# Kernel optimization log

Hardware: AMD Instinct MI355X
Metric: run time of the kernel (lower is better)

The kernel has to match this reference:

```python
import jax, jax.numpy as jnp
import numpy as np

N = 100000
D = 16          # input_dim
NUM_FILTERS = 8
NNZ = 1600000


def setup_inputs() -> dict:
    key = jax.random.key(0)
    k1, k2, k3, k4, k5 = jax.random.split(key, 5)
    x = jax.random.normal(k1, (N, D), dtype=jnp.float32)
    L_rows = jax.random.randint(k2, (NNZ,), 0, N, dtype=jnp.int64 if jax.config.jax_enable_x64 else jnp.int32).astype(jnp.int32)
    L_cols = jax.random.randint(k3, (NNZ,), 0, N, dtype=jnp.int32)
    L_v = jax.random.normal(k4, (NNZ,), dtype=jnp.float32)
    node_attr_eig = jax.random.uniform(k5, (N,), dtype=jnp.float32)
    return {"x": x, "L_rows": L_rows, "L_cols": L_cols, "L_v": L_v, "node_attr_eig": node_attr_eig}


def reference(x, L_rows, L_cols, L_v, node_attr_eig):
    n, d = x.shape
    f = NUM_FILTERS
    # exponents = 2 ** arange(num_filters + 1)
    exponents = (2 ** jnp.arange(f + 1)).astype(x.dtype)  # [F+1]
    # coeffs = x.T @ L  ==  (L.T @ x).T ; compute L.T @ x as [N, D]
    # (L.T @ x)[c] = sum over nnz entries (r, c): L_v * x[r]
    LTx = jax.ops.segment_sum(L_v[:, None] * x[L_rows], L_cols, num_segments=n)  # [N, D]
    # exponential eigenfilter bank: w = exp(-eig)^exponents, wavelet differences
    w = jnp.exp(-node_attr_eig)[:, None] ** exponents[None, :]  # [N, F+1]
    w_wav = w[:, :-1] - w[:, 1:]                                # [N, F]
    # g_eig = coeffs[..., None] * w_wav[None, ...] permuted to [N, D, F]
    g_eig = (LTx[:, :, None] * w_wav[:, None, :]).reshape(n, d * f)  # [N, D*F]
    # filtered = L @ g_eig : out[r] = sum over nnz (r, c): L_v * g_eig[c]
    out = jax.ops.segment_sum(L_v[:, None] * g_eig[L_cols], L_rows, num_segments=n)
    return out.reshape(n, d, f)
```

## Files before the change

### kernel.cpp

```cpp
#include <hip/hip_runtime.h>

#define N_NODES   100000
#define D_DIM     16
#define NFILT     8
#define KOUT      128
#define NNZ_CNT   1600000

#define CBITS     8
#define CROWS     256
#define NCB       ((N_NODES + CROWS - 1) / CROWS)
#define CAP       5120
#define EPB       4096
#define NBLKA     ((NNZ_CNT + EPB - 1) / EPB)

__device__ __forceinline__ uint f32_to_bf16_bits(float f) {
    uint u = __float_as_uint(f);
    uint r = (u + 0x7FFFu + ((u >> 16) & 1u)) >> 16;
    return r;
}

__global__ void wav_kernel(const float* __restrict__ eig, ushort* __restrict__ wavb) {
    int n = blockIdx.x * blockDim.x + threadIdx.x;
    if (n >= N_NODES) return;
    float cur = expf(-eig[n]);
    uint pk[4];
#pragma unroll
    for (int h = 0; h < 4; ++h) {
        float nx0 = cur * cur;
        float w0 = cur - nx0;
        float nx1 = nx0 * nx0;
        float w1 = nx0 - nx1;
        cur = nx1;
        pk[h] = f32_to_bf16_bits(w0) | (f32_to_bf16_bits(w1) << 16);
    }
    *(uint4*)(wavb + (size_t)n * NFILT) = make_uint4(pk[0], pk[1], pk[2], pk[3]);
}

__global__ void scatter1_kernel(const float* __restrict__ x,
                                const int* __restrict__ rows,
                                const int* __restrict__ cols,
                                const float* __restrict__ v,
                                float* __restrict__ LTxI) {
    long long idx = (long long)blockIdx.x * blockDim.x + threadIdx.x;
    if (idx >= (long long)NNZ_CNT * D_DIM) return;
    int e = (int)(idx >> 4);
    int d = (int)(idx & 15);
    int r = rows[e];
    int c = cols[e];
    float val = v[e] * x[(size_t)r * D_DIM + d];
    int slot = ((d & 7) << 1) + (d >> 3);
    atomicAdd(LTxI + (size_t)c * D_DIM + slot, val);
}

__global__ void pack_kernel(const float* __restrict__ LTxI, uint* __restrict__ LTxP) {
    int idx = blockIdx.x * blockDim.x + threadIdx.x;
    if (idx >= N_NODES * NFILT) return;
    float2 lp = *(const float2*)(LTxI + (size_t)idx * 2);
    LTxP[idx] = f32_to_bf16_bits(lp.x) | (f32_to_bf16_bits(lp.y) << 16);
}

__global__ __launch_bounds__(512) void binA_kernel(const int* __restrict__ rows,
                                                   const int* __restrict__ cols,
                                                   const float* __restrict__ v,
                                                   int* __restrict__ gcur,
                                                   int2* __restrict__ regA) {
    __shared__ int cnt[NCB];
    __shared__ int offb[NCB];
    __shared__ int gbase[NCB];
    __shared__ int sc[512];
    __shared__ int2 rec[EPB];
    int tid = threadIdx.x;
    int e0 = blockIdx.x * EPB;
    int nE = NNZ_CNT - e0; if (nE > EPB) nE = EPB;

    for (int i = tid; i < NCB; i += 512) cnt[i] = 0;
    __syncthreads();
    for (int i = tid; i < nE; i += 512)
        atomicAdd(&cnt[rows[e0 + i] >> CBITS], 1);
    __syncthreads();

    sc[tid] = (tid < NCB) ? cnt[tid] : 0;
    __syncthreads();
    for (int off = 1; off < 512; off <<= 1) {
        int t = (tid >= off) ? sc[tid - off] : 0;
        __syncthreads();
        sc[tid] += t;
        __syncthreads();
    }
    if (tid < NCB) {
        int cv = cnt[tid];
        int st = sc[tid] - cv;
        offb[tid] = st;
        gbase[tid] = cv ? atomicAdd(&gcur[tid], cv) : 0;
        cnt[tid] = st;
    }
    __syncthreads();

    for (int i = tid; i < nE; i += 512) {
        int r = rows[e0 + i], c = cols[e0 + i];
        float val = v[e0 + i];
        int b = r >> CBITS;
        int pos = atomicAdd(&cnt[b], 1);
        rec[pos] = make_int2(((r & (CROWS - 1)) << 17) | c, __float_as_int(val));
    }
    __syncthreads();

    int wv = tid >> 6, lane = tid & 63;
    for (int b = wv; b < NCB; b += 8) {
        int s = offb[b];
        int n = cnt[b] - s;
        size_t dst = (size_t)b * CAP + gbase[b];
        for (int i = lane; i < n; i += 64)
            regA[dst + i] = rec[s + i];
    }
}

__global__ __launch_bounds__(512) void binB_kernel(const int* __restrict__ gcur,
                                                   int2* __restrict__ regA,
                                                   int2* __restrict__ offs2) {
    __shared__ int2 rec[CAP];
    __shared__ int cnt[CROWS];
    __shared__ int sc[CROWS];
    int tid = threadIdx.x;
    int b = blockIdx.x;
    int nb = gcur[b]; if (nb > CAP) nb = CAP;
    size_t base = (size_t)b * CAP;

    if (tid < CROWS) cnt[tid] = 0;
    __syncthreads();
    for (int i = tid; i < nb; i += 512) {
        int2 r = regA[base + i];
        rec[i] = r;
        atomicAdd(&cnt[r.x >> 17], 1);
    }
    __syncthreads();

    int cv = (tid < CROWS) ? cnt[tid] : 0;
    if (tid < CROWS) sc[tid] = cv;
    __syncthreads();
    for (int off = 1; off < CROWS; off <<= 1) {
        int t = (tid < CROWS && tid >= off) ? sc[tid - off] : 0;
        __syncthreads();
        if (tid < CROWS) sc[tid] += t;
        __syncthreads();
    }
    if (tid < CROWS) {
        int st = sc[tid] - cv;
        int row = b * CROWS + tid;
        if (row < N_NODES)
            offs2[row] = make_int2((int)base + st, (int)base + st + cv);
        cnt[tid] = st;
    }
    __syncthreads();

    for (int i = tid; i < nb; i += 512) {
        int2 r = rec[i];
        int p = atomicAdd(&cnt[r.x >> 17], 1);
        regA[base + p] = make_int2(r.x & 0x1FFFF, r.y);
    }
}

__global__ __launch_bounds__(256) void gather2_kernel(const int2* __restrict__ offs2,
                                                      const int2* __restrict__ ep,
                                                      const uint* __restrict__ LTxP,
                                                      const ushort* __restrict__ wavb,
                                                      float* __restrict__ out) {
    int wave = (int)(((long long)blockIdx.x * blockDim.x + threadIdx.x) >> 6);
    if (wave >= N_NODES) return;
    int lane = threadIdx.x & 63;
    int r = wave;
    int d0 = lane >> 3;
    int f  = lane & 7;
    int2 se = offs2[r];
    int i = se.x, end = se.y;
    float acc0 = 0.f, acc1 = 0.f;
    for (; i + 4 <= end; i += 4) {
        int2 e0 = ep[i], e1 = ep[i + 1], e2 = ep[i + 2], e3 = ep[i + 3];
        uint l0 = LTxP[e0.x * NFILT + d0];
        uint l1 = LTxP[e1.x * NFILT + d0];
        uint l2 = LTxP[e2.x * NFILT + d0];
        uint l3 = LTxP[e3.x * NFILT + d0];
        uint w0 = wavb[e0.x * NFILT + f];
        uint w1 = wavb[e1.x * NFILT + f];
        uint w2 = wavb[e2.x * NFILT + f];
        uint w3 = wavb[e3.x * NFILT + f];
        float vw0 = __int_as_float(e0.y) * __uint_as_float(w0 << 16);
        float vw1 = __int_as_float(e1.y) * __uint_as_float(w1 << 16);
        float vw2 = __int_as_float(e2.y) * __uint_as_float(w2 << 16);
        float vw3 = __int_as_float(e3.y) * __uint_as_float(w3 << 16);
        acc0 = fmaf(vw0, __uint_as_float(l0 << 16), acc0);
        acc1 = fmaf(vw0, __uint_as_float(l0 & 0xFFFF0000u), acc1);
        acc0 = fmaf(vw1, __uint_as_float(l1 << 16), acc0);
        acc1 = fmaf(vw1, __uint_as_float(l1 & 0xFFFF0000u), acc1);
        acc0 = fmaf(vw2, __uint_as_float(l2 << 16), acc0);
        acc1 = fmaf(vw2, __uint_as_float(l2 & 0xFFFF0000u), acc1);
        acc0 = fmaf(vw3, __uint_as_float(l3 << 16), acc0);
        acc1 = fmaf(vw3, __uint_as_float(l3 & 0xFFFF0000u), acc1);
    }
    for (; i < end; ++i) {
        int2 e = ep[i];
        uint l = LTxP[e.x * NFILT + d0];
        uint w = wavb[e.x * NFILT + f];
        float vw = __int_as_float(e.y) * __uint_as_float(w << 16);
        acc0 = fmaf(vw, __uint_as_float(l << 16), acc0);
        acc1 = fmaf(vw, __uint_as_float(l & 0xFFFF0000u), acc1);
    }
    out[(size_t)r * KOUT + lane]      = acc0;
    out[(size_t)r * KOUT + 64 + lane] = acc1;
}

extern "C" void kernel_launch(void* const* d_in, const int* in_sizes, int n_in,
                              void* d_out, int out_size, void* d_ws, size_t ws_size,
                              hipStream_t stream) {
    const float* x      = (const float*)d_in[0];
    const int*   L_rows = (const int*)  d_in[1];
    const int*   L_cols = (const int*)  d_in[2];
    const float* L_v    = (const float*)d_in[3];
    const float* eig    = (const float*)d_in[4];
    float* out = (float*)d_out;

    float*  LTxI  = (float*)d_ws;
    uint*   LTxP  = (uint*)(LTxI + (size_t)N_NODES * D_DIM);
    ushort* wavb  = (ushort*)(LTxP + (size_t)N_NODES * NFILT);
    int2*   offs2 = (int2*)(wavb + (size_t)N_NODES * NFILT);
    int2*   regA  = offs2 + N_NODES;
    int*    gcur  = (int*)(regA + (size_t)NCB * CAP);

    hipMemsetAsync(LTxI, 0, (size_t)N_NODES * D_DIM * sizeof(float), stream);
    hipMemsetAsync(gcur, 0, (size_t)NCB * sizeof(int), stream);

    wav_kernel<<<(N_NODES + 255) / 256, 256, 0, stream>>>(eig, wavb);

    {
        long long total = (long long)NNZ_CNT * D_DIM;
        scatter1_kernel<<<(int)((total + 255) / 256), 256, 0, stream>>>(x, L_rows, L_cols, L_v, LTxI);
    }
    pack_kernel<<<(N_NODES * NFILT + 255) / 256, 256, 0, stream>>>(LTxI, LTxP);

    binA_kernel<<<NBLKA, 512, 0, stream>>>(L_rows, L_cols, L_v, gcur, regA);
    binB_kernel<<<NCB, 512, 0, stream>>>(gcur, regA, offs2);

    {
        long long threads = (long long)N_NODES * 64;
        gather2_kernel<<<(int)((threads + 255) / 256), 256, 0, stream>>>(offs2, regA, LTxP, wavb, out);
    }
}
```

Baseline: 278.9 us.

## Replace atomic scatter for L^T x with column-binned CSC gather

Removes the scatter1 and pack kernels, which did per-element global float atomics. Instead the existing binA/binB bucketing runs a first time keyed on columns to build a CSC layout, and a new gather1 kernel reduces each column with one wavefront and writes packed bf16 directly. This drops the LTxI memset and the atomic contention. The cost is an extra pair of binning passes over all nonzeros, with regA and offs2 reused across the two phases.

```diff
diff --git a/kernel.cpp b/kernel.cpp
--- a/kernel.cpp
+++ b/kernel.cpp
@@ -36,31 +36,8 @@
     *(uint4*)(wavb + (size_t)n * NFILT) = make_uint4(pk[0], pk[1], pk[2], pk[3]);
 }
 
-__global__ void scatter1_kernel(const float* __restrict__ x,
-                                const int* __restrict__ rows,
-                                const int* __restrict__ cols,
-                                const float* __restrict__ v,
-                                float* __restrict__ LTxI) {
-    long long idx = (long long)blockIdx.x * blockDim.x + threadIdx.x;
-    if (idx >= (long long)NNZ_CNT * D_DIM) return;
-    int e = (int)(idx >> 4);
-    int d = (int)(idx & 15);
-    int r = rows[e];
-    int c = cols[e];
-    float val = v[e] * x[(size_t)r * D_DIM + d];
-    int slot = ((d & 7) << 1) + (d >> 3);
-    atomicAdd(LTxI + (size_t)c * D_DIM + slot, val);
-}
-
-__global__ void pack_kernel(const float* __restrict__ LTxI, uint* __restrict__ LTxP) {
-    int idx = blockIdx.x * blockDim.x + threadIdx.x;
-    if (idx >= N_NODES * NFILT) return;
-    float2 lp = *(const float2*)(LTxI + (size_t)idx * 2);
-    LTxP[idx] = f32_to_bf16_bits(lp.x) | (f32_to_bf16_bits(lp.y) << 16);
-}
-
-__global__ __launch_bounds__(512) void binA_kernel(const int* __restrict__ rows,
-                                                   const int* __restrict__ cols,
+__global__ __launch_bounds__(512) void binA_kernel(const int* __restrict__ keys,
+                                                   const int* __restrict__ pays,
                                                    const float* __restrict__ v,
                                                    int* __restrict__ gcur,
                                                    int2* __restrict__ regA) {
@@ -76,7 +53,7 @@
     for (int i = tid; i < NCB; i += 512) cnt[i] = 0;
     __syncthreads();
     for (int i = tid; i < nE; i += 512)
-        atomicAdd(&cnt[rows[e0 + i] >> CBITS], 1);
+        atomicAdd(&cnt[keys[e0 + i] >> CBITS], 1);
     __syncthreads();
 
     sc[tid] = (tid < NCB) ? cnt[tid] : 0;
@@ -97,11 +74,11 @@
     __syncthreads();
 
     for (int i = tid; i < nE; i += 512) {
-        int r = rows[e0 + i], c = cols[e0 + i];
+        int k = keys[e0 + i], p = pays[e0 + i];
         float val = v[e0 + i];
-        int b = r >> CBITS;
+        int b = k >> CBITS;
         int pos = atomicAdd(&cnt[b], 1);
-        rec[pos] = make_int2(((r & (CROWS - 1)) << 17) | c, __float_as_int(val));
+        rec[pos] = make_int2(((k & (CROWS - 1)) << 17) | p, __float_as_int(val));
     }
     __syncthreads();
 
@@ -146,9 +123,9 @@
     }
     if (tid < CROWS) {
         int st = sc[tid] - cv;
-        int row = b * CROWS + tid;
-        if (row < N_NODES)
-            offs2[row] = make_int2((int)base + st, (int)base + st + cv);
+        int key = b * CROWS + tid;
+        if (key < N_NODES)
+            offs2[key] = make_int2((int)base + st, (int)base + st + cv);
         cnt[tid] = st;
     }
     __syncthreads();
@@ -158,6 +135,29 @@
         int p = atomicAdd(&cnt[r.x >> 17], 1);
         regA[base + p] = make_int2(r.x & 0x1FFFF, r.y);
     }
+}
+
+__global__ __launch_bounds__(256) void gather1_kernel(const int2* __restrict__ offs2,
+                                                      const int2* __restrict__ ep,
+                                                      const float* __restrict__ x,
+                                                      uint* __restrict__ LTxP) {
+    int wave = (int)(((long long)blockIdx.x * blockDim.x + threadIdx.x) >> 6);
+    if (wave >= N_NODES) return;
+    int lane = threadIdx.x & 63;
+    int c = wave;
+    int d = lane & 15;
+    int j = lane >> 4;
+    int2 se = offs2[c];
+    float acc = 0.f;
+    for (int i = se.x + j; i < se.y; i += 4) {
+        int2 e = ep[i];
+        acc = fmaf(__int_as_float(e.y), x[(size_t)e.x * D_DIM + d], acc);
+    }
+    acc += __shfl_xor(acc, 16);
+    acc += __shfl_xor(acc, 32);
+    float hi = __shfl_down(acc, 8);
+    if (lane < 8)
+        LTxP[(size_t)c * NFILT + lane] = f32_to_bf16_bits(acc) | (f32_to_bf16_bits(hi) << 16);
 }
 
 __global__ __launch_bounds__(256) void gather2_kernel(const int2* __restrict__ offs2,
@@ -219,27 +219,26 @@
     const float* eig    = (const float*)d_in[4];
     float* out = (float*)d_out;
 
-    float*  LTxI  = (float*)d_ws;
-    uint*   LTxP  = (uint*)(LTxI + (size_t)N_NODES * D_DIM);
+    uint*   LTxP  = (uint*)d_ws;
     ushort* wavb  = (ushort*)(LTxP + (size_t)N_NODES * NFILT);
     int2*   offs2 = (int2*)(wavb + (size_t)N_NODES * NFILT);
     int2*   regA  = offs2 + N_NODES;
     int*    gcur  = (int*)(regA + (size_t)NCB * CAP);
-
-    hipMemsetAsync(LTxI, 0, (size_t)N_NODES * D_DIM * sizeof(float), stream);
-    hipMemsetAsync(gcur, 0, (size_t)NCB * sizeof(int), stream);
+    int*    gcurB = gcur + NCB;
+
+    hipMemsetAsync(gcur, 0, (size_t)2 * NCB * sizeof(int), stream);
 
     wav_kernel<<<(N_NODES + 255) / 256, 256, 0, stream>>>(eig, wavb);
 
+    binA_kernel<<<NBLKA, 512, 0, stream>>>(L_cols, L_rows, L_v, gcurB, regA);
+    binB_kernel<<<NCB, 512, 0, stream>>>(gcurB, regA, offs2);
     {
-        long long total = (long long)NNZ_CNT * D_DIM;
-        scatter1_kernel<<<(int)((total + 255) / 256), 256, 0, stream>>>(x, L_rows, L_cols, L_v, LTxI);
-    }
-    pack_kernel<<<(N_NODES * NFILT + 255) / 256, 256, 0, stream>>>(LTxI, LTxP);
+        long long threads = (long long)N_NODES * 64;
+        gather1_kernel<<<(int)((threads + 255) / 256), 256, 0, stream>>>(offs2, regA, x, LTxP);
+    }
 
     binA_kernel<<<NBLKA, 512, 0, stream>>>(L_rows, L_cols, L_v, gcur, regA);
     binB_kernel<<<NCB, 512, 0, stream>>>(gcur, regA, offs2);
-
     {
         long long threads = (long long)N_NODES * 64;
         gather2_kernel<<<(int)((threads + 255) / 256), 256, 0, stream>>>(offs2, regA, LTxP, wavb, out);
```

New measurement: 283.5 us. About the same (+1.7%).
